# Optimization experiments

Hardware: AMD Instinct MI355X
Metric: run time of the kernel (lower is better)

Reference implementation:

```python
import jax, jax.numpy as jnp
import numpy as np

BS, LX, LY, H, MD = 16, 1024, 1024, 512, 512


def setup_inputs() -> dict:
    key = jax.random.key(0)
    ks = jax.random.split(key, 8)
    x = jax.random.normal(ks[0], (BS, LX, H), dtype=jnp.float32)
    y = jax.random.normal(ks[1], (BS, LY, H), dtype=jnp.float32)
    y_mask = jax.random.bernoulli(ks[2], 0.2, (BS, LY))  # True = masked
    s1 = 1.0 / np.sqrt(H)
    W1 = jax.random.uniform(ks[3], (MD, H), jnp.float32, -s1, s1)
    b1 = jax.random.uniform(ks[4], (MD,), jnp.float32, -s1, s1)
    W2 = jax.random.uniform(ks[5], (MD, H), jnp.float32, -s1, s1)
    b2 = jax.random.uniform(ks[6], (MD,), jnp.float32, -s1, s1)
    s2 = 1.0 / np.sqrt(MD)
    k7, k8 = jax.random.split(ks[7])
    w_o = jax.random.uniform(k7, (MD,), jnp.float32, -s2, s2)
    b_o = jax.random.uniform(k8, (), jnp.float32, -s2, s2)
    return {"x": x, "y": y, "y_mask": y_mask, "W1": W1, "b1": b1,
            "W2": W2, "b2": b2, "w_o": w_o, "b_o": b_o}


def reference(x, y, y_mask, W1, b1, W2, b2, w_o, b_o):
    # Projections: [B,L,MD]
    x_proj = jax.nn.relu(jnp.einsum('blh,mh->blm', x, W1) + b1)
    y_proj = jax.nn.relu(jnp.einsum('blh,mh->blm', y, W2) + b2)
    # o_liner is linear, so o_liner(x_i + y_j) = w_o.x_i + w_o.y_j + b_o
    sx = x_proj @ w_o  # [B,Lx]
    sy = y_proj @ w_o  # [B,Ly]
    scores = sx[:, :, None] + sy[:, None, :] + b_o  # [B,Lx,Ly]
    scores = jnp.where(y_mask[:, None, :], jnp.float32(-1e7), scores)
    alpha = jax.nn.softmax(scores, axis=-1)  # softmax over len_y
    return alpha
```

## Files before the change

kernel.cpp:

```cpp
#include <hip/hip_runtime.h>
#include <hip/hip_bf16.h>

#define BS 16
#define LX 1024
#define LY 1024
#define H 512
#define MD 512
#define RY (BS * LY)

typedef __attribute__((ext_vector_type(8))) __bf16 bf16x8;
typedef __attribute__((ext_vector_type(4))) float floatx4;

__device__ __forceinline__ void load_lds16(const __bf16* g, __bf16* l) {
    __builtin_amdgcn_global_load_lds(
        (const __attribute__((address_space(1))) void*)g,
        (__attribute__((address_space(3))) void*)l,
        16, 0, 0);
}

__global__ __launch_bounds__(256) void prep_w2(const float* __restrict__ W2,
                                               __bf16* __restrict__ wb) {
    const int i = blockIdx.x * 256 + threadIdx.x;
    const float4 a = *(const float4*)(W2 + (size_t)i * 8);
    const float4 b = *(const float4*)(W2 + (size_t)i * 8 + 4);
    bf16x8 v = { (__bf16)a.x, (__bf16)a.y, (__bf16)a.z, (__bf16)a.w,
                 (__bf16)b.x, (__bf16)b.y, (__bf16)b.z, (__bf16)b.w };
    *(bf16x8*)(wb + (size_t)i * 8) = v;
}

#define BM 64
#define BN 128
#define BKT 64
#define NK (H / BKT)
__global__ __launch_bounds__(256) void gemm_sy(const float* __restrict__ Y,
                                               const __bf16* __restrict__ wb,
                                               const float* __restrict__ b2,
                                               const float* __restrict__ wo,
                                               float* __restrict__ part) {
    __shared__ __align__(16) __bf16 Bs[2][BN * BKT];

    const int tid  = threadIdx.x;
    const int lane = tid & 63;
    const int wave = tid >> 6;
    const int wm = wave >> 1;
    const int wn = wave & 1;
    const int la = lane & 15;
    const int qa = lane >> 4;

    const int id = blockIdx.x;
    const int mt = ((id >> 5) << 3) | (id & 7);
    const int nt = (id >> 3) & 3;
    const int m0 = mt * BM, n0 = nt * BN;

    const int lrow = lane >> 3;
    const int lcol = (((lane & 7) ^ lrow) * 8);

    const float* yrow0 = Y + (size_t)(m0 + wm * 32 + la) * H + qa * 8;
    const float* yrow1 = yrow0 + 16 * H;

    floatx4 acc[2][4] = {};
    float4 a[8];

    a[0] = *(const float4*)(yrow0);      a[1] = *(const float4*)(yrow0 + 4);
    a[2] = *(const float4*)(yrow0 + 32); a[3] = *(const float4*)(yrow0 + 36);
    a[4] = *(const float4*)(yrow1);      a[5] = *(const float4*)(yrow1 + 4);
    a[6] = *(const float4*)(yrow1 + 32); a[7] = *(const float4*)(yrow1 + 36);
    #pragma unroll
    for (int r = 0; r < 4; ++r) {
        const int rb = r * 32 + wave * 8;
        load_lds16(wb + (size_t)(n0 + rb + lrow) * H + lcol, &Bs[0][rb * BKT]);
    }

    for (int k = 0; k < NK; ++k) {
        const int cur = k & 1;
        __syncthreads();

        bf16x8 afr[2][2];
        afr[0][0] = { (__bf16)a[0].x, (__bf16)a[0].y, (__bf16)a[0].z, (__bf16)a[0].w,
                      (__bf16)a[1].x, (__bf16)a[1].y, (__bf16)a[1].z, (__bf16)a[1].w };
        afr[0][1] = { (__bf16)a[2].x, (__bf16)a[2].y, (__bf16)a[2].z, (__bf16)a[2].w,
                      (__bf16)a[3].x, (__bf16)a[3].y, (__bf16)a[3].z, (__bf16)a[3].w };
        afr[1][0] = { (__bf16)a[4].x, (__bf16)a[4].y, (__bf16)a[4].z, (__bf16)a[4].w,
                      (__bf16)a[5].x, (__bf16)a[5].y, (__bf16)a[5].z, (__bf16)a[5].w };
        afr[1][1] = { (__bf16)a[6].x, (__bf16)a[6].y, (__bf16)a[6].z, (__bf16)a[6].w,
                      (__bf16)a[7].x, (__bf16)a[7].y, (__bf16)a[7].z, (__bf16)a[7].w };

        if (k + 1 < NK) {
            const int k1 = (k + 1) * BKT;
            #pragma unroll
            for (int r = 0; r < 4; ++r) {
                const int rb = r * 32 + wave * 8;
                load_lds16(wb + (size_t)(n0 + rb + lrow) * H + k1 + lcol,
                           &Bs[1 - cur][rb * BKT]);
            }
            a[0] = *(const float4*)(yrow0 + k1);      a[1] = *(const float4*)(yrow0 + k1 + 4);
            a[2] = *(const float4*)(yrow0 + k1 + 32); a[3] = *(const float4*)(yrow0 + k1 + 36);
            a[4] = *(const float4*)(yrow1 + k1);      a[5] = *(const float4*)(yrow1 + k1 + 4);
            a[6] = *(const float4*)(yrow1 + k1 + 32); a[7] = *(const float4*)(yrow1 + k1 + 36);
        }

        #pragma unroll
        for (int kh = 0; kh < 2; ++kh) {
            bf16x8 bfr[4];
            #pragma unroll
            for (int nf = 0; nf < 4; ++nf) {
                const int row  = wn * 64 + nf * 16 + la;
                const int slot = (kh * 4 + qa) ^ (la & 7);
                bfr[nf] = *(const bf16x8*)&Bs[cur][row * BKT + slot * 8];
            }
            #pragma unroll
            for (int mf = 0; mf < 2; ++mf)
                #pragma unroll
                for (int nf = 0; nf < 4; ++nf)
                    acc[mf][nf] = __builtin_amdgcn_mfma_f32_16x16x32_bf16(afr[mf][kh], bfr[nf], acc[mf][nf], 0, 0, 0);
        }
    }

    const int slice = nt * 2 + wn;
    #pragma unroll
    for (int mf = 0; mf < 2; ++mf) {
        #pragma unroll
        for (int reg = 0; reg < 4; ++reg) {
            float s = 0.f;
            #pragma unroll
            for (int nf = 0; nf < 4; ++nf) {
                const int n = n0 + wn * 64 + nf * 16 + la;
                float v = acc[mf][nf][reg] + b2[n];
                v = fmaxf(v, 0.f);
                s += v * wo[n];
            }
            s += __shfl_xor(s, 1);
            s += __shfl_xor(s, 2);
            s += __shfl_xor(s, 4);
            s += __shfl_xor(s, 8);
            if (la == 0) {
                const int m = m0 + wm * 32 + mf * 16 + qa * 4 + reg;
                part[(size_t)slice * RY + m] = s;
            }
        }
    }
}

__global__ __launch_bounds__(256) void softmax_p(const float* __restrict__ part,
                                                 const int* __restrict__ mask,
                                                 float* __restrict__ p) {
    const int b = blockIdx.x;
    const int tid = threadIdx.x;
    __shared__ float red[8];

    float vals[4];
    int   ms[4];
    float mx = -INFINITY;
    #pragma unroll
    for (int c = 0; c < 4; ++c) {
        const int j = c * 256 + tid;
        float v = 0.f;
        #pragma unroll
        for (int t = 0; t < 8; ++t) v += part[t * RY + b * LY + j];
        vals[c] = v;
        ms[c]   = mask[b * LY + j];
        if (!ms[c]) mx = fmaxf(mx, v);
    }
    #pragma unroll
    for (int off = 1; off < 64; off <<= 1) mx = fmaxf(mx, __shfl_xor(mx, off));
    if ((tid & 63) == 0) red[tid >> 6] = mx;
    __syncthreads();
    mx = fmaxf(fmaxf(red[0], red[1]), fmaxf(red[2], red[3]));

    float e[4];
    float sum = 0.f;
    #pragma unroll
    for (int c = 0; c < 4; ++c) {
        e[c] = ms[c] ? 0.f : __expf(vals[c] - mx);
        sum += e[c];
    }
    #pragma unroll
    for (int off = 1; off < 64; off <<= 1) sum += __shfl_xor(sum, off);
    if ((tid & 63) == 0) red[4 + (tid >> 6)] = sum;
    __syncthreads();
    sum = red[4] + red[5] + red[6] + red[7];
    const float inv = 1.0f / sum;

    #pragma unroll
    for (int c = 0; c < 4; ++c)
        p[b * LY + c * 256 + tid] = e[c] * inv;
}

__global__ __launch_bounds__(256) void bcast(const float* __restrict__ p,
                                             float4* __restrict__ out) {
    const int tid = threadIdx.x;
    const long base_row = (long)blockIdx.x * 8;
    const int b = (int)(base_row >> 10);
    const float4 v = *(const float4*)(p + b * LY + tid * 4);
    float4* o = out + base_row * (LY / 4) + tid;
    #pragma unroll
    for (int r = 0; r < 8; ++r) o[r * (LY / 4)] = v;
}

extern "C" void kernel_launch(void* const* d_in, const int* in_sizes, int n_in,
                              void* d_out, int out_size, void* d_ws, size_t ws_size,
                              hipStream_t stream) {
    const float* y  = (const float*)d_in[1];
    const int*   ym = (const int*)  d_in[2];
    const float* W2 = (const float*)d_in[5];
    const float* b2 = (const float*)d_in[6];
    const float* wo = (const float*)d_in[7];

    char* ws = (char*)d_ws;
    __bf16* wb   = (__bf16*)ws;
    float*  part = (float*)(ws + (size_t)MD * H * 2);
    float*  p    = part + 8 * RY;

    prep_w2<<<(MD * H) / (256 * 8), 256, 0, stream>>>(W2, wb);
    gemm_sy<<<(MD / BN) * (RY / BM), 256, 0, stream>>>(y, wb, b2, wo, part);
    softmax_p<<<BS, 256, 0, stream>>>(part, ym, p);
    bcast<<<(BS * LX) / 8, 256, 0, stream>>>(p, (float4*)d_out);
}
```

Baseline: 165.1 us.

## Preload full-K W2 slice into LDS once and retile GEMM to 128x64

The GEMM tile changes from 64x128 to 128x64. Each block now loads its whole 64-row, full-K bf16 W2 slice (64KB) into LDS once, with an XOR swizzle, instead of double-buffering K chunks with a barrier per iteration. The four waves each own 32 rows of M and all 64 N columns, which removes the per-iteration __syncthreads and the B reloads. The cost is a larger LDS footprint that limits blocks per CU (launch bounds ask for 2), and an exposed initial B load that is no longer overlapped with compute.

```diff
diff --git a/kernel.cpp b/kernel.cpp
--- a/kernel.cpp
+++ b/kernel.cpp
@@ -28,34 +28,37 @@
     *(bf16x8*)(wb + (size_t)i * 8) = v;
 }
 
-#define BM 64
-#define BN 128
+#define BM 128
+#define BN 64
 #define BKT 64
 #define NK (H / BKT)
-__global__ __launch_bounds__(256) void gemm_sy(const float* __restrict__ Y,
-                                               const __bf16* __restrict__ wb,
-                                               const float* __restrict__ b2,
-                                               const float* __restrict__ wo,
-                                               float* __restrict__ part) {
-    __shared__ __align__(16) __bf16 Bs[2][BN * BKT];
+__global__ __launch_bounds__(256, 2) void gemm_sy(const float* __restrict__ Y,
+                                                  const __bf16* __restrict__ wb,
+                                                  const float* __restrict__ b2,
+                                                  const float* __restrict__ wo,
+                                                  float* __restrict__ part) {
+    __shared__ __align__(16) __bf16 Bs[BN * H];
 
     const int tid  = threadIdx.x;
     const int lane = tid & 63;
     const int wave = tid >> 6;
-    const int wm = wave >> 1;
-    const int wn = wave & 1;
     const int la = lane & 15;
     const int qa = lane >> 4;
 
     const int id = blockIdx.x;
-    const int mt = ((id >> 5) << 3) | (id & 7);
-    const int nt = (id >> 3) & 3;
+    const int mt = ((id >> 6) << 3) | (id & 7);
+    const int nt = (id >> 3) & 7;
     const int m0 = mt * BM, n0 = nt * BN;
 
-    const int lrow = lane >> 3;
-    const int lcol = (((lane & 7) ^ lrow) * 8);
-
-    const float* yrow0 = Y + (size_t)(m0 + wm * 32 + la) * H + qa * 8;
+    #pragma unroll
+    for (int r = 0; r < 16; ++r) {
+        const int row = wave * 16 + r;
+        const int g   = lane ^ (row & 7);
+        load_lds16(wb + (size_t)(n0 + row) * H + g * 8, &Bs[row * H]);
+    }
+    __syncthreads();
+
+    const float* yrow0 = Y + (size_t)(m0 + wave * 32 + la) * H + qa * 8;
     const float* yrow1 = yrow0 + 16 * H;
 
     floatx4 acc[2][4] = {};
@@ -65,16 +68,8 @@
     a[2] = *(const float4*)(yrow0 + 32); a[3] = *(const float4*)(yrow0 + 36);
     a[4] = *(const float4*)(yrow1);      a[5] = *(const float4*)(yrow1 + 4);
     a[6] = *(const float4*)(yrow1 + 32); a[7] = *(const float4*)(yrow1 + 36);
-    #pragma unroll
-    for (int r = 0; r < 4; ++r) {
-        const int rb = r * 32 + wave * 8;
-        load_lds16(wb + (size_t)(n0 + rb + lrow) * H + lcol, &Bs[0][rb * BKT]);
-    }
 
     for (int k = 0; k < NK; ++k) {
-        const int cur = k & 1;
-        __syncthreads();
-
         bf16x8 afr[2][2];
         afr[0][0] = { (__bf16)a[0].x, (__bf16)a[0].y, (__bf16)a[0].z, (__bf16)a[0].w,
                       (__bf16)a[1].x, (__bf16)a[1].y, (__bf16)a[1].z, (__bf16)a[1].w };
@@ -87,26 +82,21 @@
 
         if (k + 1 < NK) {
             const int k1 = (k + 1) * BKT;
-            #pragma unroll
-            for (int r = 0; r < 4; ++r) {
-                const int rb = r * 32 + wave * 8;
-                load_lds16(wb + (size_t)(n0 + rb + lrow) * H + k1 + lcol,
-                           &Bs[1 - cur][rb * BKT]);
-            }
             a[0] = *(const float4*)(yrow0 + k1);      a[1] = *(const float4*)(yrow0 + k1 + 4);
             a[2] = *(const float4*)(yrow0 + k1 + 32); a[3] = *(const float4*)(yrow0 + k1 + 36);
             a[4] = *(const float4*)(yrow1 + k1);      a[5] = *(const float4*)(yrow1 + k1 + 4);
             a[6] = *(const float4*)(yrow1 + k1 + 32); a[7] = *(const float4*)(yrow1 + k1 + 36);
         }
 
+        const int gbase = k * (BKT / 8);
         #pragma unroll
         for (int kh = 0; kh < 2; ++kh) {
             bf16x8 bfr[4];
             #pragma unroll
             for (int nf = 0; nf < 4; ++nf) {
-                const int row  = wn * 64 + nf * 16 + la;
-                const int slot = (kh * 4 + qa) ^ (la & 7);
-                bfr[nf] = *(const bf16x8*)&Bs[cur][row * BKT + slot * 8];
+                const int row  = nf * 16 + la;
+                const int slot = (gbase + kh * 4 + qa) ^ (la & 7);
+                bfr[nf] = *(const bf16x8*)&Bs[row * H + slot * 8];
             }
             #pragma unroll
             for (int mf = 0; mf < 2; ++mf)
@@ -116,7 +106,6 @@
         }
     }
 
-    const int slice = nt * 2 + wn;
     #pragma unroll
     for (int mf = 0; mf < 2; ++mf) {
         #pragma unroll
@@ -124,7 +113,7 @@
             float s = 0.f;
             #pragma unroll
             for (int nf = 0; nf < 4; ++nf) {
-                const int n = n0 + wn * 64 + nf * 16 + la;
+                const int n = n0 + nf * 16 + la;
                 float v = acc[mf][nf][reg] + b2[n];
                 v = fmaxf(v, 0.f);
                 s += v * wo[n];
@@ -134,8 +123,8 @@
             s += __shfl_xor(s, 4);
             s += __shfl_xor(s, 8);
             if (la == 0) {
-                const int m = m0 + wm * 32 + mf * 16 + qa * 4 + reg;
-                part[(size_t)slice * RY + m] = s;
+                const int m = m0 + wave * 32 + mf * 16 + qa * 4 + reg;
+                part[(size_t)nt * RY + m] = s;
             }
         }
     }
```

Result: faster. 157.8 us (-4.5%).
